# Kernel tuning notes

Measured on AMD Instinct MI355X. Metric: run time of the kernel, lower is better.

Reference implementation:

```python
import jax, jax.numpy as jnp
import numpy as np

N_NODES = 100000
N_EDGES = 6400000
D_FEAT = 128

def setup_inputs() -> dict:
    key = jax.random.key(0)
    k1, k2, k3 = jax.random.split(key, 3)
    h = jax.random.normal(k1, (N_NODES, D_FEAT), dtype=jnp.float32)
    src = jax.random.randint(k2, (N_EDGES,), 0, N_NODES, dtype=jnp.int64)
    dst = jax.random.randint(k3, (N_EDGES,), 0, N_NODES, dtype=jnp.int64)
    return {"h": h, "src": src, "dst": dst}

def reference(h, src, dst):
    N = h.shape[0]
    pos = h[:, 0]                                  # [N] scalar position per node
    # per-edge message: |pos_src - pos_dst|
    dist = jnp.abs(pos[src] - pos[dst])            # [E]
    # segment-mean over incoming edges at each dst node
    s = jax.ops.segment_sum(dist, dst, num_segments=N)                  # [N]
    cnt = jax.ops.segment_sum(jnp.ones_like(dist), dst, num_segments=N)  # [N] in-degree
    h_dst = s / jnp.maximum(cnt, 1.0)              # zero-in-degree nodes -> 0 (DGL default)
    return jnp.stack([pos, h_dst], axis=1)         # [N, 2]
```

## Files before the change

kernel.cpp:

```cpp
#include <hip/hip_runtime.h>
#include <hip/hip_fp16.h>

#define D_FEAT 128
#define NBINS_MAX 10
#define BIN_SIZE 10000
#define PB 2000
#define PB_THREADS 256
#define CAP 512
#define CAP_SHIFT 9
#define SBB 25
#define SEGS (PB / SBB)
#define SC_THREADS 1024
#define DIST_SCALE 1024.0f
#define INV_DIST_SCALE (1.0f / 1024.0f)

__global__ void init_pos(const float* __restrict__ h, float* __restrict__ pos,
                         unsigned short* __restrict__ posh, int n) {
    int i = blockIdx.x * blockDim.x + threadIdx.x;
    if (i < n) {
        float v = h[(size_t)i * D_FEAT];
        pos[i] = v;
        posh[i] = __half_as_ushort(__float2half(v));
    }
}

__global__ __launch_bounds__(PB_THREADS, 8) void prep_kernel(
        const int* __restrict__ src, const int* __restrict__ dst,
        const unsigned short* __restrict__ posh,
        unsigned int* __restrict__ pv2, unsigned int* __restrict__ cnts,
        int n_edges, int nbins, int chunk) {
    __shared__ unsigned int cursor[NBINS_MAX];
    const int b = blockIdx.x;
    const int t = threadIdx.x;
    if (t < nbins) cursor[t] = 0u;
    __syncthreads();

    const long base = (long)b * chunk;
    long lim = (long)n_edges - base;
    if (lim > chunk) lim = chunk;
    if (lim < 0) lim = 0;

#define PREP_ONE(dd, hh)                                                        \
    {                                                                           \
        unsigned int d = (unsigned int)(dd);                                    \
        unsigned int bin = d / BIN_SIZE;                                        \
        unsigned int drel = d - bin * BIN_SIZE;                                 \
        unsigned int slot = atomicAdd(&cursor[bin], 1u);                        \
        if (slot < CAP) {                                                       \
            unsigned int off = ((bin * PB + (unsigned int)b) << CAP_SHIFT) + slot; \
            __builtin_nontemporal_store(((unsigned int)(hh) << 14) | drel,      \
                                        pv2 + off);                             \
        }                                                                       \
    }

    const long R = (lim / (PB_THREADS * 12)) * (PB_THREADS * 12);
    for (long k0 = (long)t * 12; k0 < R; k0 += PB_THREADS * 12) {
        const int* dp = dst + base + k0;
        const int* sp = src + base + k0;
        int4 da = *(const int4*)dp;
        int4 db = *(const int4*)(dp + 4);
        int4 dc = *(const int4*)(dp + 8);
        int4 sa = *(const int4*)sp;
        int4 sb = *(const int4*)(sp + 4);
        int4 sc = *(const int4*)(sp + 8);
        unsigned short a0 = posh[sa.x];
        unsigned short a1 = posh[sa.y];
        unsigned short a2 = posh[sa.z];
        unsigned short a3 = posh[sa.w];
        unsigned short a4 = posh[sb.x];
        unsigned short a5 = posh[sb.y];
        unsigned short a6 = posh[sb.z];
        unsigned short a7 = posh[sb.w];
        unsigned short a8 = posh[sc.x];
        unsigned short a9 = posh[sc.y];
        unsigned short a10 = posh[sc.z];
        unsigned short a11 = posh[sc.w];
        PREP_ONE(da.x, a0);
        PREP_ONE(da.y, a1);
        PREP_ONE(da.z, a2);
        PREP_ONE(da.w, a3);
        PREP_ONE(db.x, a4);
        PREP_ONE(db.y, a5);
        PREP_ONE(db.z, a6);
        PREP_ONE(db.w, a7);
        PREP_ONE(dc.x, a8);
        PREP_ONE(dc.y, a9);
        PREP_ONE(dc.z, a10);
        PREP_ONE(dc.w, a11);
    }
    for (long k = R + t; k < lim; k += PB_THREADS) {
        unsigned short a = posh[src[base + k]];
        PREP_ONE(dst[base + k], a);
    }
#undef PREP_ONE
    __syncthreads();
    if (t < nbins) {
        unsigned int c = cursor[t];
        cnts[t * PB + b] = c < CAP ? c : CAP;
    }
}

__global__ __launch_bounds__(SC_THREADS) void scatter_kernel(
        const unsigned int* __restrict__ pv2, const unsigned int* __restrict__ cnts,
        const float* __restrict__ pos, unsigned int* __restrict__ part,
        int n_nodes) {
    __shared__ unsigned int lacc[BIN_SIZE];
    __shared__ float pos_lds[BIN_SIZE];
    __shared__ unsigned int cl[SEGS];
    const int bx = blockIdx.x;
    const int bin = bx / SBB;
    const int j = bx - bin * SBB;
    const int bin_lo = bin * BIN_SIZE;
    const int bin_n = min(BIN_SIZE, n_nodes - bin_lo);
    const int t = threadIdx.x;

    if (t < SEGS) cl[t] = cnts[bin * PB + j * SEGS + t];
    for (int k = t; k < bin_n; k += SC_THREADS) {
        lacc[k] = 0u;
        pos_lds[k] = pos[bin_lo + k];
    }
    __syncthreads();

#define SC_BODY(vv)                                                             \
    {                                                                           \
        float a = __half2float(__ushort_as_half((unsigned short)((vv) >> 14))); \
        unsigned int r = (vv) & 0x3FFFu;                                        \
        unsigned int f = min((unsigned int)(fabsf(a - pos_lds[r]) * DIST_SCALE + 0.5f), 16383u); \
        atomicAdd(&lacc[r], (1u << 24) | f);                                    \
    }

    const unsigned int* pj = pv2 + (((size_t)bin * PB + (size_t)j * SEGS) << CAP_SHIFT);
    const int TOT = SEGS * CAP;
    for (int idx = t * 8; idx < TOT; idx += SC_THREADS * 8) {
        int seg = idx >> CAP_SHIFT;
        int slot = idx & (CAP - 1);
        int cnt = (int)cl[seg];
        const unsigned int* p = pj + ((size_t)seg << CAP_SHIFT);
        if (slot + 8 <= cnt) {
            uint4 va = *(const uint4*)(p + slot);
            uint4 vb = *(const uint4*)(p + slot + 4);
            SC_BODY(va.x); SC_BODY(va.y); SC_BODY(va.z); SC_BODY(va.w);
            SC_BODY(vb.x); SC_BODY(vb.y); SC_BODY(vb.z); SC_BODY(vb.w);
        } else if (slot < cnt) {
            for (int q = slot; q < cnt && q < slot + 8; ++q) SC_BODY(p[q]);
        }
    }
#undef SC_BODY
    __syncthreads();

    unsigned int* slice = part + (size_t)j * n_nodes + bin_lo;
    for (int k = t; k < bin_n; k += SC_THREADS) slice[k] = lacc[k];
}

__global__ void merge_kernel(const float* __restrict__ pos,
                             const unsigned int* __restrict__ part,
                             float* __restrict__ out, int n_nodes) {
    int i0 = (blockIdx.x * blockDim.x + threadIdx.x) * 4;
    if (i0 + 4 <= n_nodes) {
        unsigned int c0 = 0, c1 = 0, c2 = 0, c3 = 0;
        unsigned int s0 = 0, s1 = 0, s2 = 0, s3 = 0;
        for (int b = 0; b < SBB; ++b) {
            uint4 p = *(const uint4*)(part + (size_t)b * n_nodes + i0);
            c0 += p.x >> 24; s0 += p.x & 0x00FFFFFFu;
            c1 += p.y >> 24; s1 += p.y & 0x00FFFFFFu;
            c2 += p.z >> 24; s2 += p.z & 0x00FFFFFFu;
            c3 += p.w >> 24; s3 += p.w & 0x00FFFFFFu;
        }
        float4 ps = *(const float4*)(pos + i0);
        float4 oa, ob;
        oa.x = ps.x; oa.y = ((float)s0 * INV_DIST_SCALE) / fmaxf((float)c0, 1.0f);
        oa.z = ps.y; oa.w = ((float)s1 * INV_DIST_SCALE) / fmaxf((float)c1, 1.0f);
        ob.x = ps.z; ob.y = ((float)s2 * INV_DIST_SCALE) / fmaxf((float)c2, 1.0f);
        ob.z = ps.w; ob.w = ((float)s3 * INV_DIST_SCALE) / fmaxf((float)c3, 1.0f);
        ((float4*)out)[(i0 >> 1)] = oa;
        ((float4*)out)[(i0 >> 1) + 1] = ob;
    } else {
        for (int i = i0; i < n_nodes; ++i) {
            unsigned int cnt = 0, sum = 0;
            for (int b = 0; b < SBB; ++b) {
                unsigned int p = part[(size_t)b * n_nodes + i];
                cnt += p >> 24;
                sum += p & 0x00FFFFFFu;
            }
            float2 o;
            o.x = pos[i];
            o.y = ((float)sum * INV_DIST_SCALE) / fmaxf((float)cnt, 1.0f);
            ((float2*)out)[i] = o;
        }
    }
}

__global__ void fb_init(const float* __restrict__ h, float* __restrict__ pos,
                        unsigned long long* __restrict__ acc, int n) {
    int i = blockIdx.x * blockDim.x + threadIdx.x;
    if (i < n) { pos[i] = h[(size_t)i * D_FEAT]; acc[i] = 0ull; }
}
__global__ void fb_edge(const int* __restrict__ src, const int* __restrict__ dst,
                        const float* __restrict__ pos,
                        unsigned long long* __restrict__ acc, int n_edges) {
    int stride = gridDim.x * blockDim.x;
    for (int i = blockIdx.x * blockDim.x + threadIdx.x; i < n_edges; i += stride) {
        float dist = fabsf(pos[src[i]] - pos[dst[i]]);
        unsigned int fx = (unsigned int)(dist * 262144.0f + 0.5f);
        atomicAdd(&acc[dst[i]], (1ull << 32) | (unsigned long long)fx);
    }
}
__global__ void fb_final(const float* __restrict__ pos,
                         const unsigned long long* __restrict__ acc,
                         float* __restrict__ out, int n) {
    int i = blockIdx.x * blockDim.x + threadIdx.x;
    if (i < n) {
        unsigned long long v = acc[i];
        unsigned int cnt = (unsigned int)(v >> 32);
        float s = (float)(unsigned int)(v & 0xffffffffull) * (1.0f / 262144.0f);
        float2 o; o.x = pos[i]; o.y = s / fmaxf((float)cnt, 1.0f);
        ((float2*)out)[i] = o;
    }
}

extern "C" void kernel_launch(void* const* d_in, const int* in_sizes, int n_in,
                              void* d_out, int out_size, void* d_ws, size_t ws_size,
                              hipStream_t stream) {
    const float* h = (const float*)d_in[0];
    const int* src = (const int*)d_in[1];
    const int* dst = (const int*)d_in[2];
    float* out = (float*)d_out;

    int n_nodes = in_sizes[0] / D_FEAT;
    int n_edges = in_sizes[1];

    int chunk = (n_edges + PB - 1) / PB;
    int nbins = (n_nodes + BIN_SIZE - 1) / BIN_SIZE;
    size_t pos_bytes  = ((size_t)n_nodes * 4 + 255) & ~(size_t)255;
    size_t posh_bytes = ((size_t)n_nodes * 2 + 255) & ~(size_t)255;
    size_t pv2_bytes  = (((size_t)nbins * PB << CAP_SHIFT) * 4 + 255) & ~(size_t)255;
    size_t cnts_bytes = ((size_t)nbins * PB * 4 + 255) & ~(size_t)255;
    size_t part_bytes = (size_t)SBB * n_nodes * 4;
    bool fast_ok = (ws_size >= pos_bytes + posh_bytes + pv2_bytes + cnts_bytes + part_bytes) &&
                   (n_nodes <= (1 << 17)) && (nbins <= NBINS_MAX) &&
                   ((size_t)chunk * 10 <= (size_t)CAP * nbins * 7);

    int block = 256;
    int ngrid = (n_nodes + block - 1) / block;

    if (fast_ok) {
        char* w = (char*)d_ws;
        float* pos = (float*)w;                          w += pos_bytes;
        unsigned short* posh = (unsigned short*)w;       w += posh_bytes;
        unsigned int* pv2 = (unsigned int*)w;            w += pv2_bytes;
        unsigned int* cnts = (unsigned int*)w;           w += cnts_bytes;
        unsigned int* part = (unsigned int*)w;
        init_pos<<<ngrid, block, 0, stream>>>(h, pos, posh, n_nodes);
        prep_kernel<<<PB, PB_THREADS, 0, stream>>>(src, dst, posh, pv2, cnts,
                                                   n_edges, nbins, chunk);
        scatter_kernel<<<nbins * SBB, SC_THREADS, 0, stream>>>(pv2, cnts, pos,
                                                               part, n_nodes);
        int mgrid = (n_nodes + block * 4 - 1) / (block * 4);
        merge_kernel<<<mgrid, block, 0, stream>>>(pos, part, out, n_nodes);
    } else {
        float* pos = (float*)d_ws;
        unsigned long long* acc = (unsigned long long*)((char*)d_ws + pos_bytes);
        fb_init<<<ngrid, block, 0, stream>>>(h, pos, acc, n_nodes);
        fb_edge<<<(n_edges + block - 1) / block, block, 0, stream>>>(src, dst, pos, acc, n_edges);
        fb_final<<<ngrid, block, 0, stream>>>(pos, acc, out, n_nodes);
    }
}
```

Measured before the change: 183.9 us.

## Stage binned edges in LDS and defer source-position gather to scatter

The prep kernel now packs the raw source index with the relative destination, writes it into a per-block shared-memory bin buffer, and flushes each bin to global memory with coalesced 16-byte stores instead of scattered per-edge nontemporal stores. The half-precision position gather by source index moves from prep into the scatter kernel. The aim is cleaner write traffic in prep and no dependent random loads ahead of the binning atomics. In exchange prep uses about 20KB of LDS per block, which may cut occupancy, and the random posh gathers now sit in scatter's inner loop.

```diff
diff --git a/kernel.cpp b/kernel.cpp
--- a/kernel.cpp
+++ b/kernel.cpp
@@ -8,6 +8,7 @@
 #define PB_THREADS 256
 #define CAP 512
 #define CAP_SHIFT 9
+#define LBSTRIDE (CAP + 4)
 #define SBB 25
 #define SEGS (PB / SBB)
 #define SC_THREADS 1024
@@ -26,10 +27,10 @@
 
 __global__ __launch_bounds__(PB_THREADS, 8) void prep_kernel(
         const int* __restrict__ src, const int* __restrict__ dst,
-        const unsigned short* __restrict__ posh,
         unsigned int* __restrict__ pv2, unsigned int* __restrict__ cnts,
         int n_edges, int nbins, int chunk) {
     __shared__ unsigned int cursor[NBINS_MAX];
+    __shared__ __align__(16) unsigned int lbin[NBINS_MAX * LBSTRIDE];
     const int b = blockIdx.x;
     const int t = threadIdx.x;
     if (t < nbins) cursor[t] = 0u;
@@ -40,17 +41,14 @@
     if (lim > chunk) lim = chunk;
     if (lim < 0) lim = 0;
 
-#define PREP_ONE(dd, hh)                                                        \
+#define PREP_ONE(dd, ss)                                                        \
     {                                                                           \
         unsigned int d = (unsigned int)(dd);                                    \
         unsigned int bin = d / BIN_SIZE;                                        \
         unsigned int drel = d - bin * BIN_SIZE;                                 \
         unsigned int slot = atomicAdd(&cursor[bin], 1u);                        \
-        if (slot < CAP) {                                                       \
-            unsigned int off = ((bin * PB + (unsigned int)b) << CAP_SHIFT) + slot; \
-            __builtin_nontemporal_store(((unsigned int)(hh) << 14) | drel,      \
-                                        pv2 + off);                             \
-        }                                                                       \
+        if (slot < CAP)                                                         \
+            lbin[bin * LBSTRIDE + slot] = ((unsigned int)(ss) << 14) | drel;    \
     }
 
     const long R = (lim / (PB_THREADS * 12)) * (PB_THREADS * 12);
@@ -63,47 +61,38 @@
         int4 sa = *(const int4*)sp;
         int4 sb = *(const int4*)(sp + 4);
         int4 sc = *(const int4*)(sp + 8);
-        unsigned short a0 = posh[sa.x];
-        unsigned short a1 = posh[sa.y];
-        unsigned short a2 = posh[sa.z];
-        unsigned short a3 = posh[sa.w];
-        unsigned short a4 = posh[sb.x];
-        unsigned short a5 = posh[sb.y];
-        unsigned short a6 = posh[sb.z];
-        unsigned short a7 = posh[sb.w];
-        unsigned short a8 = posh[sc.x];
-        unsigned short a9 = posh[sc.y];
-        unsigned short a10 = posh[sc.z];
-        unsigned short a11 = posh[sc.w];
-        PREP_ONE(da.x, a0);
-        PREP_ONE(da.y, a1);
-        PREP_ONE(da.z, a2);
-        PREP_ONE(da.w, a3);
-        PREP_ONE(db.x, a4);
-        PREP_ONE(db.y, a5);
-        PREP_ONE(db.z, a6);
-        PREP_ONE(db.w, a7);
-        PREP_ONE(dc.x, a8);
-        PREP_ONE(dc.y, a9);
-        PREP_ONE(dc.z, a10);
-        PREP_ONE(dc.w, a11);
+        PREP_ONE(da.x, sa.x);
+        PREP_ONE(da.y, sa.y);
+        PREP_ONE(da.z, sa.z);
+        PREP_ONE(da.w, sa.w);
+        PREP_ONE(db.x, sb.x);
+        PREP_ONE(db.y, sb.y);
+        PREP_ONE(db.z, sb.z);
+        PREP_ONE(db.w, sb.w);
+        PREP_ONE(dc.x, sc.x);
+        PREP_ONE(dc.y, sc.y);
+        PREP_ONE(dc.z, sc.z);
+        PREP_ONE(dc.w, sc.w);
     }
     for (long k = R + t; k < lim; k += PB_THREADS) {
-        unsigned short a = posh[src[base + k]];
-        PREP_ONE(dst[base + k], a);
+        PREP_ONE(dst[base + k], src[base + k]);
     }
 #undef PREP_ONE
     __syncthreads();
-    if (t < nbins) {
-        unsigned int c = cursor[t];
-        cnts[t * PB + b] = c < CAP ? c : CAP;
-    }
+
+    for (int bin = 0; bin < nbins; ++bin) {
+        int cnt = (int)min(cursor[bin], (unsigned int)CAP);
+        unsigned int* op = pv2 + (((size_t)bin * PB + b) << CAP_SHIFT);
+        for (int w = t * 4; w < cnt; w += PB_THREADS * 4)
+            *(uint4*)(op + w) = *(const uint4*)&lbin[bin * LBSTRIDE + w];
+    }
+    if (t < nbins) cnts[t * PB + b] = min(cursor[t], (unsigned int)CAP);
 }
 
 __global__ __launch_bounds__(SC_THREADS) void scatter_kernel(
         const unsigned int* __restrict__ pv2, const unsigned int* __restrict__ cnts,
-        const float* __restrict__ pos, unsigned int* __restrict__ part,
-        int n_nodes) {
+        const float* __restrict__ pos, const unsigned short* __restrict__ posh,
+        unsigned int* __restrict__ part, int n_nodes) {
     __shared__ unsigned int lacc[BIN_SIZE];
     __shared__ float pos_lds[BIN_SIZE];
     __shared__ unsigned int cl[SEGS];
@@ -121,9 +110,9 @@
     }
     __syncthreads();
 
-#define SC_BODY(vv)                                                             \
+#define SC_BODY(vv, hh)                                                         \
     {                                                                           \
-        float a = __half2float(__ushort_as_half((unsigned short)((vv) >> 14))); \
+        float a = __half2float(__ushort_as_half((unsigned short)(hh)));         \
         unsigned int r = (vv) & 0x3FFFu;                                        \
         unsigned int f = min((unsigned int)(fabsf(a - pos_lds[r]) * DIST_SCALE + 0.5f), 16383u); \
         atomicAdd(&lacc[r], (1u << 24) | f);                                    \
@@ -139,10 +128,21 @@
         if (slot + 8 <= cnt) {
             uint4 va = *(const uint4*)(p + slot);
             uint4 vb = *(const uint4*)(p + slot + 4);
-            SC_BODY(va.x); SC_BODY(va.y); SC_BODY(va.z); SC_BODY(va.w);
-            SC_BODY(vb.x); SC_BODY(vb.y); SC_BODY(vb.z); SC_BODY(vb.w);
+            unsigned short h0 = posh[va.x >> 14];
+            unsigned short h1 = posh[va.y >> 14];
+            unsigned short h2 = posh[va.z >> 14];
+            unsigned short h3 = posh[va.w >> 14];
+            unsigned short h4 = posh[vb.x >> 14];
+            unsigned short h5 = posh[vb.y >> 14];
+            unsigned short h6 = posh[vb.z >> 14];
+            unsigned short h7 = posh[vb.w >> 14];
+            SC_BODY(va.x, h0); SC_BODY(va.y, h1); SC_BODY(va.z, h2); SC_BODY(va.w, h3);
+            SC_BODY(vb.x, h4); SC_BODY(vb.y, h5); SC_BODY(vb.z, h6); SC_BODY(vb.w, h7);
         } else if (slot < cnt) {
-            for (int q = slot; q < cnt && q < slot + 8; ++q) SC_BODY(p[q]);
+            for (int q = slot; q < cnt && q < slot + 8; ++q) {
+                unsigned int v = p[q];
+                SC_BODY(v, posh[v >> 14]);
+            }
         }
     }
 #undef SC_BODY
@@ -251,9 +251,9 @@
         unsigned int* cnts = (unsigned int*)w;           w += cnts_bytes;
         unsigned int* part = (unsigned int*)w;
         init_pos<<<ngrid, block, 0, stream>>>(h, pos, posh, n_nodes);
-        prep_kernel<<<PB, PB_THREADS, 0, stream>>>(src, dst, posh, pv2, cnts,
+        prep_kernel<<<PB, PB_THREADS, 0, stream>>>(src, dst, pv2, cnts,
                                                    n_edges, nbins, chunk);
-        scatter_kernel<<<nbins * SBB, SC_THREADS, 0, stream>>>(pv2, cnts, pos,
+        scatter_kernel<<<nbins * SBB, SC_THREADS, 0, stream>>>(pv2, cnts, pos, posh,
                                                                part, n_nodes);
         int mgrid = (n_nodes + block * 4 - 1) / (block * 4);
         merge_kernel<<<mgrid, block, 0, stream>>>(pos, part, out, n_nodes);
```

Result: faster. 165.9 us (-9.8%).
